# Kernel tuning notes

Measured on AMD Instinct MI355X. Metric: run time of the kernel, lower is better.

The kernel has to match this reference:

```python
import jax, jax.numpy as jnp
import numpy as np

INPUT_DIM = 512
PROJ_DIM = 128
HIDDEN = INPUT_DIM // 2  # 256


def setup_inputs() -> dict:
    key = jax.random.key(0)
    ks = jax.random.split(key, 6)
    B = 8192
    s1 = 1.0 / np.sqrt(INPUT_DIM)
    s2 = 1.0 / np.sqrt(HIDDEN)
    return {
        "fused_text": jax.random.normal(ks[0], (B, INPUT_DIM), dtype=jnp.float32),
        "x": jax.random.normal(ks[1], (B, INPUT_DIM), dtype=jnp.float32),
        # generator layer 1: Linear(input_dim, input_dim//2), torch layout [out, in]
        "W1": jax.random.uniform(ks[2], (HIDDEN, INPUT_DIM), jnp.float32, -s1, s1),
        "b1": jax.random.uniform(ks[3], (HIDDEN,), jnp.float32, -s1, s1),
        # generator layer 2: Linear(input_dim//2, proj_dim * input_dim)
        "W2": jax.random.uniform(ks[4], (PROJ_DIM * INPUT_DIM, HIDDEN), jnp.float32, -s2, s2),
        "b2": jax.random.uniform(ks[5], (PROJ_DIM * INPUT_DIM,), jnp.float32, -s2, s2),
    }


def reference(fused_text, x, W1, b1, W2, b2):
    B = fused_text.shape[0]
    # hypernetwork generator MLP
    h = jax.nn.relu(fused_text @ W1.T + b1)          # [B, hidden]
    w_flat = h @ W2.T + b2                           # [B, proj_dim * input_dim]
    W = w_flat.reshape(B, PROJ_DIM, INPUT_DIM)       # per-sample weights
    # per-sample projection: bmm(W, x[..., None]).squeeze(-1)
    out = jnp.einsum("bpi,bi->bp", W, x)             # [B, proj_dim]
    return out
```

## Files before the change

### kernel.cpp

```cpp
#include <hip/hip_runtime.h>
#include <stdint.h>

#define B_SZ   8192
#define IN_DIM 512
#define HID    256
#define PROJ   128

typedef __attribute__((ext_vector_type(8))) short bf16x8;
typedef __attribute__((ext_vector_type(4))) float f32x4;

#define GLDS16(gp, lp) __builtin_amdgcn_global_load_lds( \
    (const __attribute__((address_space(1))) void*)(gp), \
    (__attribute__((address_space(3))) void*)(lp), 16, 0, 0)

__device__ __forceinline__ unsigned short f2bf(float f) {
    union { float f; uint32_t u; } c; c.f = f;
    uint32_t u = c.u;
    uint32_t r = (u + 0x7fffu + ((u >> 16) & 1u)) >> 16;
    return (unsigned short)r;
}
__device__ __forceinline__ float bfhi(uint32_t v) {
    union { uint32_t u; float f; } c; c.u = v & 0xffff0000u; return c.f;
}
__device__ __forceinline__ float bflo(uint32_t v) {
    union { uint32_t u; float f; } c; c.u = v << 16; return c.f;
}

__global__ __launch_bounds__(256) void k0_prep(
        const float4* __restrict__ W2, ushort4* __restrict__ W2b,
        const float* __restrict__ x, unsigned short* __restrict__ xTb) {
    __shared__ float tile[64][65];
    const int bid = blockIdx.x;
    if (bid < 2048) {
        const int nW2 = (PROJ * IN_DIM * HID) / 4;
        const int stride = 2048 * 256;
        for (int i = bid * 256 + threadIdx.x; i < nW2; i += stride) {
            float4 v = W2[i];
            ushort4 o;
            o.x = f2bf(v.x); o.y = f2bf(v.y); o.z = f2bf(v.z); o.w = f2bf(v.w);
            W2b[i] = o;
        }
    } else {
        const int tb = bid - 2048;
        const int bi = tb & 7, bb = tb >> 3;
        const int i0 = bi * 64, b0 = bb * 64;
        const int t = threadIdx.x;
        const int c = t & 63, r4 = t >> 6;
        #pragma unroll
        for (int rr = 0; rr < 64; rr += 4)
            tile[rr + r4][c] = x[(size_t)(b0 + rr + r4) * IN_DIM + i0 + c];
        __syncthreads();
        #pragma unroll
        for (int rr = 0; rr < 64; rr += 4)
            xTb[(size_t)(i0 + rr + r4) * B_SZ + b0 + c] = f2bf(tile[c][rr + r4]);
    }
}

__device__ __forceinline__ bf16x8 ld_cvt8(const float* __restrict__ s) {
    float4 a = *(const float4*)s;
    float4 b = *(const float4*)(s + 4);
    bf16x8 r;
    r[0] = (short)f2bf(a.x); r[1] = (short)f2bf(a.y);
    r[2] = (short)f2bf(a.z); r[3] = (short)f2bf(a.w);
    r[4] = (short)f2bf(b.x); r[5] = (short)f2bf(b.y);
    r[6] = (short)f2bf(b.z); r[7] = (short)f2bf(b.w);
    return r;
}

__global__ __launch_bounds__(256) void k1_hidden(
        const float* __restrict__ ft,
        const float* __restrict__ W1,
        const float* __restrict__ b1,
        unsigned short* __restrict__ hb) {
    const int lane = threadIdx.x & 63;
    const int wv   = threadIdx.x >> 6;
    const int l15  = lane & 15, q = lane >> 4;
    const int b0 = blockIdx.x * 64;
    const int n0 = wv * 64;

    f32x4 acc[4][4];
    const f32x4 z4 = {0.f, 0.f, 0.f, 0.f};
    #pragma unroll
    for (int mt = 0; mt < 4; ++mt)
        #pragma unroll
        for (int nt = 0; nt < 4; ++nt) acc[mt][nt] = z4;

    for (int kq = 0; kq < 16; ++kq) {
        const int koff = kq * 32 + q * 8;
        bf16x8 a[4], bb[4];
        #pragma unroll
        for (int mt = 0; mt < 4; ++mt)
            a[mt] = ld_cvt8(ft + (size_t)(b0 + mt*16 + l15) * IN_DIM + koff);
        #pragma unroll
        for (int nt = 0; nt < 4; ++nt)
            bb[nt] = ld_cvt8(W1 + (size_t)(n0 + nt*16 + l15) * IN_DIM + koff);
        #pragma unroll
        for (int mt = 0; mt < 4; ++mt)
            #pragma unroll
            for (int nt = 0; nt < 4; ++nt)
                acc[mt][nt] = __builtin_amdgcn_mfma_f32_16x16x32_bf16(
                    a[mt], bb[nt], acc[mt][nt], 0, 0, 0);
    }
    #pragma unroll
    for (int nt = 0; nt < 4; ++nt) {
        float bias = b1[n0 + nt*16 + l15];
        #pragma unroll
        for (int mt = 0; mt < 4; ++mt)
            #pragma unroll
            for (int r = 0; r < 4; ++r) {
                float v = acc[mt][nt][r] + bias;
                v = fmaxf(v, 0.f);
                hb[(size_t)(b0 + mt*16 + q*4 + r) * HID + n0 + nt*16 + l15] = f2bf(v);
            }
    }
}

__global__ __launch_bounds__(256, 4) void k3_main(
        const unsigned short* __restrict__ W2b,
        const unsigned short* __restrict__ hb,
        const unsigned short* __restrict__ xTb,
        const float* __restrict__ b2,
        float* __restrict__ out) {
    __shared__ unsigned short lbs[2][64 * 128];
    const int tid  = threadIdx.x;
    const int lane = tid & 63;
    const int wv   = tid >> 6;
    const int l15  = lane & 15, q = lane >> 4;
    const int pgrp = blockIdx.x & 63;
    const int bsup = blockIdx.x >> 6;
    const int p0   = pgrp * 2;
    const int b0w  = bsup * 128 + wv * 32;
    const f32x4 z4 = {0.f, 0.f, 0.f, 0.f};

    const int grow_sub = lane >> 4;
    const int cbase    = (lane & 15) ^ grow_sub;

    const int qx   = q ^ (l15 & 3);
    const int kbit = (l15 >> 2) & 1;

    float oacc[2][2][4];
    #pragma unroll
    for (int pp = 0; pp < 2; ++pp)
        #pragma unroll
        for (int mt = 0; mt < 2; ++mt)
            #pragma unroll
            for (int r = 0; r < 4; ++r) oacc[pp][mt][r] = 0.f;

    bf16x8 afr[2][4];

    {
        #pragma unroll
        for (int jj = 0; jj < 4; ++jj) {
            const int j   = wv * 4 + jj;
            const int row = j * 4 + grow_sub;
            const int p   = row >> 5, ir = row & 31;
            const int c   = cbase ^ (4 * (jj & 1));
            const unsigned short* g = W2b
                + ((size_t)(p0 + p) * IN_DIM + ir) * HID + c * 8;
            GLDS16(g, &lbs[0][j * 512]);
        }
    }

    #pragma unroll 1
    for (int t = 0; t < 32; ++t) {
        __syncthreads();

        if (t < 31) {
            const int tn = t + 1;
            const int kh = tn >> 4, i0 = (tn & 15) * 32;
            unsigned short* Ld = lbs[tn & 1];
            #pragma unroll
            for (int jj = 0; jj < 4; ++jj) {
                const int j   = wv * 4 + jj;
                const int row = j * 4 + grow_sub;
                const int p   = row >> 5, ir = row & 31;
                const int c   = cbase ^ (4 * (jj & 1));
                const unsigned short* g = W2b
                    + ((size_t)(p0 + p) * IN_DIM + i0 + ir) * HID + kh * 128 + c * 8;
                GLDS16(g, &Ld[j * 512]);
            }
        }

        const int kh = t >> 4;
        if ((t & 15) == 0) {
            #pragma unroll
            for (int mt = 0; mt < 2; ++mt) {
                const unsigned short* hrow =
                    hb + (size_t)(b0w + mt*16 + l15) * HID + kh * 128 + q * 8;
                #pragma unroll
                for (int kq = 0; kq < 4; ++kq)
                    afr[mt][kq] = *(const bf16x8*)(hrow + kq * 32);
            }
        }

        const unsigned short* Lb = lbs[t & 1];
        const int i0 = (t & 15) * 32;

        #pragma unroll
        for (int sub = 0; sub < 2; ++sub) {
            const int irow = i0 + sub * 16 + l15;
            uint2 xv[2];
            const unsigned short* xp = xTb + (size_t)irow * B_SZ + b0w + q * 4;
            #pragma unroll
            for (int mt = 0; mt < 2; ++mt)
                xv[mt] = *(const uint2*)(xp + mt * 16);

            const float b2v = (kh == 0) ? b2[p0 * 512 + irow] : 0.f;
            const float b2w = (kh == 0) ? b2[(p0 + 1) * 512 + irow] : 0.f;

            #pragma unroll
            for (int pp = 0; pp < 2; ++pp) {
                const unsigned short* Bp = Lb + (pp*32 + sub*16 + l15) * 128;
                bf16x8 bfr[4];
                #pragma unroll
                for (int kq = 0; kq < 4; ++kq) {
                    const int cpos = qx + 4 * (kq ^ kbit);
                    bfr[kq] = *(const bf16x8*)(Bp + cpos * 8);
                }

                f32x4 D[2];
                #pragma unroll
                for (int mt = 0; mt < 2; ++mt)
                    D[mt] = __builtin_amdgcn_mfma_f32_16x16x32_bf16(afr[mt][0], bfr[0], z4, 0, 0, 0);
                #pragma unroll
                for (int kq = 1; kq < 4; ++kq)
                    #pragma unroll
                    for (int mt = 0; mt < 2; ++mt)
                        D[mt] = __builtin_amdgcn_mfma_f32_16x16x32_bf16(afr[mt][kq], bfr[kq], D[mt], 0, 0, 0);

                const float bb = pp ? b2w : b2v;
                #pragma unroll
                for (int mt = 0; mt < 2; ++mt) {
                    oacc[pp][mt][0] = fmaf(D[mt][0] + bb, bflo(xv[mt].x), oacc[pp][mt][0]);
                    oacc[pp][mt][1] = fmaf(D[mt][1] + bb, bfhi(xv[mt].x), oacc[pp][mt][1]);
                    oacc[pp][mt][2] = fmaf(D[mt][2] + bb, bflo(xv[mt].y), oacc[pp][mt][2]);
                    oacc[pp][mt][3] = fmaf(D[mt][3] + bb, bfhi(xv[mt].y), oacc[pp][mt][3]);
                }
            }
        }
    }

    #pragma unroll
    for (int pp = 0; pp < 2; ++pp)
        #pragma unroll
        for (int mt = 0; mt < 2; ++mt)
            #pragma unroll
            for (int r = 0; r < 4; ++r) {
                float v = oacc[pp][mt][r];
                v += __shfl_xor(v, 1, 16);
                v += __shfl_xor(v, 2, 16);
                v += __shfl_xor(v, 4, 16);
                v += __shfl_xor(v, 8, 16);
                if (l15 == 0)
                    out[(size_t)(b0w + mt*16 + q*4 + r) * PROJ + p0 + pp] = v;
            }
}

extern "C" void kernel_launch(void* const* d_in, const int* in_sizes, int n_in,
                              void* d_out, int out_size, void* d_ws, size_t ws_size,
                              hipStream_t stream) {
    const float* ft = (const float*)d_in[0];
    const float* x  = (const float*)d_in[1];
    const float* W1 = (const float*)d_in[2];
    const float* b1 = (const float*)d_in[3];
    const float* W2 = (const float*)d_in[4];
    const float* b2 = (const float*)d_in[5];
    float* out = (float*)d_out;

    char* ws = (char*)d_ws;
    unsigned short* W2b = (unsigned short*)(ws);
    unsigned short* hb  = (unsigned short*)(ws + 33554432);
    unsigned short* xTb = (unsigned short*)(ws + 37748736);

    hipLaunchKernelGGL(k0_prep, dim3(3072), dim3(256), 0, stream,
        (const float4*)W2, (ushort4*)W2b, x, xTb);
    hipLaunchKernelGGL(k1_hidden, dim3(128), dim3(256), 0, stream, ft, W1, b1, hb);
    hipLaunchKernelGGL(k3_main, dim3(4096), dim3(256), 0, stream, W2b, hb, xTb, b2, out);
}
```

Baseline: 489.3 us.

## Hoist b2 bias term into separate x·B2 GEMM and enlarge main kernel batch tile

The b2 bias contribution is factored out algebraically as x @ reshape(b2, PROJ, IN_DIM)^T and computed by a new small MFMA kernel that writes the output first. The main kernel then accumulates into out with +=, dropping the per-row bias loads and adds. The main kernel's per-wave batch tile is doubled from 32 to 64 rows, with occupancy hint lowered from 4 to 3 and half the blocks, to reuse each LDS-staged W2 tile across more samples. k1 is also retiled to 32 rows per block with twice the grid. The trade is more registers per thread and an extra launch, plus a read-modify-write of out.

```diff
diff --git a/kernel.cpp b/kernel.cpp
--- a/kernel.cpp
+++ b/kernel.cpp
@@ -75,27 +75,27 @@
     const int lane = threadIdx.x & 63;
     const int wv   = threadIdx.x >> 6;
     const int l15  = lane & 15, q = lane >> 4;
-    const int b0 = blockIdx.x * 64;
+    const int b0 = blockIdx.x * 32;
     const int n0 = wv * 64;
 
-    f32x4 acc[4][4];
+    f32x4 acc[2][4];
     const f32x4 z4 = {0.f, 0.f, 0.f, 0.f};
     #pragma unroll
-    for (int mt = 0; mt < 4; ++mt)
+    for (int mt = 0; mt < 2; ++mt)
         #pragma unroll
         for (int nt = 0; nt < 4; ++nt) acc[mt][nt] = z4;
 
     for (int kq = 0; kq < 16; ++kq) {
         const int koff = kq * 32 + q * 8;
-        bf16x8 a[4], bb[4];
-        #pragma unroll
-        for (int mt = 0; mt < 4; ++mt)
+        bf16x8 a[2], bb[4];
+        #pragma unroll
+        for (int mt = 0; mt < 2; ++mt)
             a[mt] = ld_cvt8(ft + (size_t)(b0 + mt*16 + l15) * IN_DIM + koff);
         #pragma unroll
         for (int nt = 0; nt < 4; ++nt)
             bb[nt] = ld_cvt8(W1 + (size_t)(n0 + nt*16 + l15) * IN_DIM + koff);
         #pragma unroll
-        for (int mt = 0; mt < 4; ++mt)
+        for (int mt = 0; mt < 2; ++mt)
             #pragma unroll
             for (int nt = 0; nt < 4; ++nt)
                 acc[mt][nt] = __builtin_amdgcn_mfma_f32_16x16x32_bf16(
@@ -105,7 +105,7 @@
     for (int nt = 0; nt < 4; ++nt) {
         float bias = b1[n0 + nt*16 + l15];
         #pragma unroll
-        for (int mt = 0; mt < 4; ++mt)
+        for (int mt = 0; mt < 2; ++mt)
             #pragma unroll
             for (int r = 0; r < 4; ++r) {
                 float v = acc[mt][nt][r] + bias;
@@ -115,11 +115,53 @@
     }
 }
 
-__global__ __launch_bounds__(256, 4) void k3_main(
+__global__ __launch_bounds__(256) void k2_bias(
+        const float* __restrict__ x,
+        const float* __restrict__ b2,
+        float* __restrict__ out) {
+    const int lane = threadIdx.x & 63;
+    const int wv   = threadIdx.x >> 6;
+    const int l15  = lane & 15, q = lane >> 4;
+    const int b0 = blockIdx.x * 32;
+    const int n0 = wv * 32;
+
+    f32x4 acc[2][2];
+    const f32x4 z4 = {0.f, 0.f, 0.f, 0.f};
+    #pragma unroll
+    for (int mt = 0; mt < 2; ++mt)
+        #pragma unroll
+        for (int nt = 0; nt < 2; ++nt) acc[mt][nt] = z4;
+
+    for (int kq = 0; kq < 16; ++kq) {
+        const int koff = kq * 32 + q * 8;
+        bf16x8 a[2], bb[2];
+        #pragma unroll
+        for (int mt = 0; mt < 2; ++mt)
+            a[mt] = ld_cvt8(x + (size_t)(b0 + mt*16 + l15) * IN_DIM + koff);
+        #pragma unroll
+        for (int nt = 0; nt < 2; ++nt)
+            bb[nt] = ld_cvt8(b2 + (size_t)(n0 + nt*16 + l15) * IN_DIM + koff);
+        #pragma unroll
+        for (int mt = 0; mt < 2; ++mt)
+            #pragma unroll
+            for (int nt = 0; nt < 2; ++nt)
+                acc[mt][nt] = __builtin_amdgcn_mfma_f32_16x16x32_bf16(
+                    a[mt], bb[nt], acc[mt][nt], 0, 0, 0);
+    }
+    #pragma unroll
+    for (int mt = 0; mt < 2; ++mt)
+        #pragma unroll
+        for (int nt = 0; nt < 2; ++nt)
+            #pragma unroll
+            for (int r = 0; r < 4; ++r)
+                out[(size_t)(b0 + mt*16 + q*4 + r) * PROJ + n0 + nt*16 + l15]
+                    = acc[mt][nt][r];
+}
+
+__global__ __launch_bounds__(256, 3) void k3_main(
         const unsigned short* __restrict__ W2b,
         const unsigned short* __restrict__ hb,
         const unsigned short* __restrict__ xTb,
-        const float* __restrict__ b2,
         float* __restrict__ out) {
     __shared__ unsigned short lbs[2][64 * 128];
     const int tid  = threadIdx.x;
@@ -129,7 +171,7 @@
     const int pgrp = blockIdx.x & 63;
     const int bsup = blockIdx.x >> 6;
     const int p0   = pgrp * 2;
-    const int b0w  = bsup * 128 + wv * 32;
+    const int b0w  = bsup * 256 + wv * 64;
     const f32x4 z4 = {0.f, 0.f, 0.f, 0.f};
 
     const int grow_sub = lane >> 4;
@@ -138,15 +180,15 @@
     const int qx   = q ^ (l15 & 3);
     const int kbit = (l15 >> 2) & 1;
 
-    float oacc[2][2][4];
+    float oacc[2][4][4];
     #pragma unroll
     for (int pp = 0; pp < 2; ++pp)
         #pragma unroll
-        for (int mt = 0; mt < 2; ++mt)
+        for (int mt = 0; mt < 4; ++mt)
             #pragma unroll
             for (int r = 0; r < 4; ++r) oacc[pp][mt][r] = 0.f;
 
-    bf16x8 afr[2][4];
+    bf16x8 afr[4][4];
 
     {
         #pragma unroll
@@ -184,7 +226,7 @@
         const int kh = t >> 4;
         if ((t & 15) == 0) {
             #pragma unroll
-            for (int mt = 0; mt < 2; ++mt) {
+            for (int mt = 0; mt < 4; ++mt) {
                 const unsigned short* hrow =
                     hb + (size_t)(b0w + mt*16 + l15) * HID + kh * 128 + q * 8;
                 #pragma unroll
@@ -199,14 +241,11 @@
         #pragma unroll
         for (int sub = 0; sub < 2; ++sub) {
             const int irow = i0 + sub * 16 + l15;
-            uint2 xv[2];
+            uint2 xv[4];
             const unsigned short* xp = xTb + (size_t)irow * B_SZ + b0w + q * 4;
             #pragma unroll
-            for (int mt = 0; mt < 2; ++mt)
+            for (int mt = 0; mt < 4; ++mt)
                 xv[mt] = *(const uint2*)(xp + mt * 16);
-
-            const float b2v = (kh == 0) ? b2[p0 * 512 + irow] : 0.f;
-            const float b2w = (kh == 0) ? b2[(p0 + 1) * 512 + irow] : 0.f;
 
             #pragma unroll
             for (int pp = 0; pp < 2; ++pp) {
@@ -218,23 +257,22 @@
                     bfr[kq] = *(const bf16x8*)(Bp + cpos * 8);
                 }
 
-                f32x4 D[2];
-                #pragma unroll
-                for (int mt = 0; mt < 2; ++mt)
+                f32x4 D[4];
+                #pragma unroll
+                for (int mt = 0; mt < 4; ++mt)
                     D[mt] = __builtin_amdgcn_mfma_f32_16x16x32_bf16(afr[mt][0], bfr[0], z4, 0, 0, 0);
                 #pragma unroll
                 for (int kq = 1; kq < 4; ++kq)
                     #pragma unroll
-                    for (int mt = 0; mt < 2; ++mt)
+                    for (int mt = 0; mt < 4; ++mt)
                         D[mt] = __builtin_amdgcn_mfma_f32_16x16x32_bf16(afr[mt][kq], bfr[kq], D[mt], 0, 0, 0);
 
-                const float bb = pp ? b2w : b2v;
-                #pragma unroll
-                for (int mt = 0; mt < 2; ++mt) {
-                    oacc[pp][mt][0] = fmaf(D[mt][0] + bb, bflo(xv[mt].x), oacc[pp][mt][0]);
-                    oacc[pp][mt][1] = fmaf(D[mt][1] + bb, bfhi(xv[mt].x), oacc[pp][mt][1]);
-                    oacc[pp][mt][2] = fmaf(D[mt][2] + bb, bflo(xv[mt].y), oacc[pp][mt][2]);
-                    oacc[pp][mt][3] = fmaf(D[mt][3] + bb, bfhi(xv[mt].y), oacc[pp][mt][3]);
+                #pragma unroll
+                for (int mt = 0; mt < 4; ++mt) {
+                    oacc[pp][mt][0] = fmaf(D[mt][0], bflo(xv[mt].x), oacc[pp][mt][0]);
+                    oacc[pp][mt][1] = fmaf(D[mt][1], bfhi(xv[mt].x), oacc[pp][mt][1]);
+                    oacc[pp][mt][2] = fmaf(D[mt][2], bflo(xv[mt].y), oacc[pp][mt][2]);
+                    oacc[pp][mt][3] = fmaf(D[mt][3], bfhi(xv[mt].y), oacc[pp][mt][3]);
                 }
             }
         }
@@ -243,7 +281,7 @@
     #pragma unroll
     for (int pp = 0; pp < 2; ++pp)
         #pragma unroll
-        for (int mt = 0; mt < 2; ++mt)
+        for (int mt = 0; mt < 4; ++mt)
             #pragma unroll
             for (int r = 0; r < 4; ++r) {
                 float v = oacc[pp][mt][r];
@@ -251,8 +289,11 @@
                 v += __shfl_xor(v, 2, 16);
                 v += __shfl_xor(v, 4, 16);
                 v += __shfl_xor(v, 8, 16);
-                if (l15 == 0)
-                    out[(size_t)(b0w + mt*16 + q*4 + r) * PROJ + p0 + pp] = v;
+                if (l15 == 0) {
+                    const size_t idx =
+                        (size_t)(b0w + mt*16 + q*4 + r) * PROJ + p0 + pp;
+                    out[idx] += v;
+                }
             }
 }
 
@@ -274,6 +315,7 @@
 
     hipLaunchKernelGGL(k0_prep, dim3(3072), dim3(256), 0, stream,
         (const float4*)W2, (ushort4*)W2b, x, xTb);
-    hipLaunchKernelGGL(k1_hidden, dim3(128), dim3(256), 0, stream, ft, W1, b1, hb);
-    hipLaunchKernelGGL(k3_main, dim3(4096), dim3(256), 0, stream, W2b, hb, xTb, b2, out);
-}
+    hipLaunchKernelGGL(k1_hidden, dim3(256), dim3(256), 0, stream, ft, W1, b1, hb);
+    hipLaunchKernelGGL(k2_bias, dim3(256), dim3(256), 0, stream, x, b2, out);
+    hipLaunchKernelGGL(k3_main, dim3(2048), dim3(256), 0, stream, W2b, hb, xTb, out);
+}
```

Result: slower. 654.8 us (+33.8%).

## Factor b2 term into separate GEMM, retile main kernel, drop x transpose

Applied to the files above, without the earlier changes.

Splits the bias contribution b2·x out of the main loop into a small MFMA GEMM (k2_bias) that writes a transposed output buffer. The main kernel then accumulates into that buffer, and a final kernel transposes it to [B, PROJ]. The main kernel now covers 128 batch rows per wave with a 64-wide k chunk, and reads fp32 x directly instead of a pre-transposed bf16 copy, so the x transpose in prep goes away. This adds two kernel launches and a read-modify-write of outT. Occupancy drops to 3 blocks per SM, and the afr/xq register arrays are larger.

```diff
diff --git a/kernel.cpp b/kernel.cpp
--- a/kernel.cpp
+++ b/kernel.cpp
@@ -19,40 +19,16 @@
     uint32_t r = (u + 0x7fffu + ((u >> 16) & 1u)) >> 16;
     return (unsigned short)r;
 }
-__device__ __forceinline__ float bfhi(uint32_t v) {
-    union { uint32_t u; float f; } c; c.u = v & 0xffff0000u; return c.f;
-}
-__device__ __forceinline__ float bflo(uint32_t v) {
-    union { uint32_t u; float f; } c; c.u = v << 16; return c.f;
-}
 
 __global__ __launch_bounds__(256) void k0_prep(
-        const float4* __restrict__ W2, ushort4* __restrict__ W2b,
-        const float* __restrict__ x, unsigned short* __restrict__ xTb) {
-    __shared__ float tile[64][65];
-    const int bid = blockIdx.x;
-    if (bid < 2048) {
-        const int nW2 = (PROJ * IN_DIM * HID) / 4;
-        const int stride = 2048 * 256;
-        for (int i = bid * 256 + threadIdx.x; i < nW2; i += stride) {
-            float4 v = W2[i];
-            ushort4 o;
-            o.x = f2bf(v.x); o.y = f2bf(v.y); o.z = f2bf(v.z); o.w = f2bf(v.w);
-            W2b[i] = o;
-        }
-    } else {
-        const int tb = bid - 2048;
-        const int bi = tb & 7, bb = tb >> 3;
-        const int i0 = bi * 64, b0 = bb * 64;
-        const int t = threadIdx.x;
-        const int c = t & 63, r4 = t >> 6;
-        #pragma unroll
-        for (int rr = 0; rr < 64; rr += 4)
-            tile[rr + r4][c] = x[(size_t)(b0 + rr + r4) * IN_DIM + i0 + c];
-        __syncthreads();
-        #pragma unroll
-        for (int rr = 0; rr < 64; rr += 4)
-            xTb[(size_t)(i0 + rr + r4) * B_SZ + b0 + c] = f2bf(tile[c][rr + r4]);
+        const float4* __restrict__ W2, ushort4* __restrict__ W2b) {
+    const int nW2 = (PROJ * IN_DIM * HID) / 4;
+    const int stride = 2048 * 256;
+    for (int i = blockIdx.x * 256 + threadIdx.x; i < nW2; i += stride) {
+        float4 v = W2[i];
+        ushort4 o;
+        o.x = f2bf(v.x); o.y = f2bf(v.y); o.z = f2bf(v.z); o.w = f2bf(v.w);
+        W2b[i] = o;
     }
 }
 
@@ -75,27 +51,27 @@
     const int lane = threadIdx.x & 63;
     const int wv   = threadIdx.x >> 6;
     const int l15  = lane & 15, q = lane >> 4;
-    const int b0 = blockIdx.x * 64;
+    const int b0 = blockIdx.x * 32;
     const int n0 = wv * 64;
 
-    f32x4 acc[4][4];
+    f32x4 acc[2][4];
     const f32x4 z4 = {0.f, 0.f, 0.f, 0.f};
     #pragma unroll
-    for (int mt = 0; mt < 4; ++mt)
+    for (int mt = 0; mt < 2; ++mt)
         #pragma unroll
         for (int nt = 0; nt < 4; ++nt) acc[mt][nt] = z4;
 
     for (int kq = 0; kq < 16; ++kq) {
         const int koff = kq * 32 + q * 8;
-        bf16x8 a[4], bb[4];
-        #pragma unroll
-        for (int mt = 0; mt < 4; ++mt)
+        bf16x8 a[2], bb[4];
+        #pragma unroll
+        for (int mt = 0; mt < 2; ++mt)
             a[mt] = ld_cvt8(ft + (size_t)(b0 + mt*16 + l15) * IN_DIM + koff);
         #pragma unroll
         for (int nt = 0; nt < 4; ++nt)
             bb[nt] = ld_cvt8(W1 + (size_t)(n0 + nt*16 + l15) * IN_DIM + koff);
         #pragma unroll
-        for (int mt = 0; mt < 4; ++mt)
+        for (int mt = 0; mt < 2; ++mt)
             #pragma unroll
             for (int nt = 0; nt < 4; ++nt)
                 acc[mt][nt] = __builtin_amdgcn_mfma_f32_16x16x32_bf16(
@@ -105,7 +81,7 @@
     for (int nt = 0; nt < 4; ++nt) {
         float bias = b1[n0 + nt*16 + l15];
         #pragma unroll
-        for (int mt = 0; mt < 4; ++mt)
+        for (int mt = 0; mt < 2; ++mt)
             #pragma unroll
             for (int r = 0; r < 4; ++r) {
                 float v = acc[mt][nt][r] + bias;
@@ -115,13 +91,55 @@
     }
 }
 
-__global__ __launch_bounds__(256, 4) void k3_main(
+__global__ __launch_bounds__(256) void k2_bias(
+        const float* __restrict__ x,
+        const float* __restrict__ b2,
+        float* __restrict__ outT) {
+    const int lane = threadIdx.x & 63;
+    const int wv   = threadIdx.x >> 6;
+    const int l15  = lane & 15, q = lane >> 4;
+    const int b0 = blockIdx.x * 64;
+    const int pw = wv * 32;
+
+    f32x4 acc[2][4];
+    const f32x4 z4 = {0.f, 0.f, 0.f, 0.f};
+    #pragma unroll
+    for (int pt = 0; pt < 2; ++pt)
+        #pragma unroll
+        for (int bb = 0; bb < 4; ++bb) acc[pt][bb] = z4;
+
+    for (int kq = 0; kq < 16; ++kq) {
+        const int koff = kq * 32 + q * 8;
+        bf16x8 a[2], bx[4];
+        #pragma unroll
+        for (int pt = 0; pt < 2; ++pt)
+            a[pt] = ld_cvt8(b2 + (size_t)(pw + pt*16 + l15) * IN_DIM + koff);
+        #pragma unroll
+        for (int bb = 0; bb < 4; ++bb)
+            bx[bb] = ld_cvt8(x + (size_t)(b0 + bb*16 + l15) * IN_DIM + koff);
+        #pragma unroll
+        for (int pt = 0; pt < 2; ++pt)
+            #pragma unroll
+            for (int bb = 0; bb < 4; ++bb)
+                acc[pt][bb] = __builtin_amdgcn_mfma_f32_16x16x32_bf16(
+                    a[pt], bx[bb], acc[pt][bb], 0, 0, 0);
+    }
+    #pragma unroll
+    for (int pt = 0; pt < 2; ++pt)
+        #pragma unroll
+        for (int bb = 0; bb < 4; ++bb)
+            #pragma unroll
+            for (int r = 0; r < 4; ++r)
+                outT[(size_t)(pw + pt*16 + q*4 + r) * B_SZ + b0 + bb*16 + l15]
+                    = acc[pt][bb][r];
+}
+
+__global__ __launch_bounds__(256, 3) void k3_main(
         const unsigned short* __restrict__ W2b,
         const unsigned short* __restrict__ hb,
-        const unsigned short* __restrict__ xTb,
-        const float* __restrict__ b2,
-        float* __restrict__ out) {
-    __shared__ unsigned short lbs[2][64 * 128];
+        const float* __restrict__ x,
+        float* __restrict__ outT) {
+    __shared__ unsigned short lbs[2][64 * 64];
     const int tid  = threadIdx.x;
     const int lane = tid & 63;
     const int wv   = tid >> 6;
@@ -129,112 +147,87 @@
     const int pgrp = blockIdx.x & 63;
     const int bsup = blockIdx.x >> 6;
     const int p0   = pgrp * 2;
-    const int b0w  = bsup * 128 + wv * 32;
+    const int b0w  = bsup * 512 + wv * 128;
     const f32x4 z4 = {0.f, 0.f, 0.f, 0.f};
 
-    const int grow_sub = lane >> 4;
-    const int cbase    = (lane & 15) ^ grow_sub;
-
-    const int qx   = q ^ (l15 & 3);
-    const int kbit = (l15 >> 2) & 1;
-
-    float oacc[2][2][4];
+    const int grow = lane >> 3;
+    const int gchk = lane & 7;
+
+    const unsigned short* gsrc[2];
+    #pragma unroll
+    for (int jj = 0; jj < 2; ++jj) {
+        const int r = wv*16 + jj*8 + grow;
+        const int c = gchk ^ (r & 7);
+        gsrc[jj] = W2b + ((size_t)(p0 + (r >> 5)) * IN_DIM + (r & 31)) * HID + c * 8;
+    }
+
+    float oacc[2][8];
     #pragma unroll
     for (int pp = 0; pp < 2; ++pp)
         #pragma unroll
-        for (int mt = 0; mt < 2; ++mt)
-            #pragma unroll
-            for (int r = 0; r < 4; ++r) oacc[pp][mt][r] = 0.f;
-
-    bf16x8 afr[2][4];
-
-    {
-        #pragma unroll
-        for (int jj = 0; jj < 4; ++jj) {
-            const int j   = wv * 4 + jj;
-            const int row = j * 4 + grow_sub;
-            const int p   = row >> 5, ir = row & 31;
-            const int c   = cbase ^ (4 * (jj & 1));
-            const unsigned short* g = W2b
-                + ((size_t)(p0 + p) * IN_DIM + ir) * HID + c * 8;
-            GLDS16(g, &lbs[0][j * 512]);
-        }
-    }
+        for (int bt = 0; bt < 8; ++bt) oacc[pp][bt] = 0.f;
+
+    bf16x8 afr[8][2];
+
+    const unsigned short* hbase = hb + (size_t)(b0w + l15) * HID + q * 8;
+    const float* xbase = x + (size_t)(b0w + l15) * IN_DIM + q * 4;
+
+    #pragma unroll
+    for (int jj = 0; jj < 2; ++jj)
+        GLDS16(gsrc[jj], &lbs[0][(wv*16 + jj*8) * 64]);
 
     #pragma unroll 1
-    for (int t = 0; t < 32; ++t) {
+    for (int t = 0; t < 64; ++t) {
         __syncthreads();
 
-        if (t < 31) {
+        if (t < 63) {
             const int tn = t + 1;
-            const int kh = tn >> 4, i0 = (tn & 15) * 32;
+            const int khn = tn >> 4, icn = tn & 15;
             unsigned short* Ld = lbs[tn & 1];
             #pragma unroll
-            for (int jj = 0; jj < 4; ++jj) {
-                const int j   = wv * 4 + jj;
-                const int row = j * 4 + grow_sub;
-                const int p   = row >> 5, ir = row & 31;
-                const int c   = cbase ^ (4 * (jj & 1));
-                const unsigned short* g = W2b
-                    + ((size_t)(p0 + p) * IN_DIM + i0 + ir) * HID + kh * 128 + c * 8;
-                GLDS16(g, &Ld[j * 512]);
+            for (int jj = 0; jj < 2; ++jj)
+                GLDS16(gsrc[jj] + (size_t)icn * 32 * HID + khn * 64,
+                       &Ld[(wv*16 + jj*8) * 64]);
+        }
+
+        const int kh = t >> 4;
+        const int ic = t & 15;
+        if ((t & 15) == 0) {
+            #pragma unroll
+            for (int bt = 0; bt < 8; ++bt) {
+                const unsigned short* hrow = hbase + bt * 16 * HID + kh * 64;
+                afr[bt][0] = *(const bf16x8*)(hrow);
+                afr[bt][1] = *(const bf16x8*)(hrow + 32);
             }
         }
 
-        const int kh = t >> 4;
-        if ((t & 15) == 0) {
-            #pragma unroll
-            for (int mt = 0; mt < 2; ++mt) {
-                const unsigned short* hrow =
-                    hb + (size_t)(b0w + mt*16 + l15) * HID + kh * 128 + q * 8;
+        const unsigned short* Lb = lbs[t & 1];
+
+        #pragma unroll
+        for (int sub = 0; sub < 2; ++sub) {
+            float4 xq[8];
+            #pragma unroll
+            for (int bt = 0; bt < 8; ++bt)
+                xq[bt] = *(const float4*)(xbase + (size_t)bt * 16 * IN_DIM
+                                          + ic * 32 + sub * 16);
+            #pragma unroll
+            for (int pp = 0; pp < 2; ++pp) {
+                const int trow = pp*32 + sub*16 + l15;
+                const int sw = trow & 7;
+                bf16x8 wf0 = *(const bf16x8*)(&Lb[trow*64 + ((q)     ^ sw) * 8]);
+                bf16x8 wf1 = *(const bf16x8*)(&Lb[trow*64 + ((4 + q) ^ sw) * 8]);
                 #pragma unroll
-                for (int kq = 0; kq < 4; ++kq)
-                    afr[mt][kq] = *(const bf16x8*)(hrow + kq * 32);
-            }
-        }
-
-        const unsigned short* Lb = lbs[t & 1];
-        const int i0 = (t & 15) * 32;
-
-        #pragma unroll
-        for (int sub = 0; sub < 2; ++sub) {
-            const int irow = i0 + sub * 16 + l15;
-            uint2 xv[2];
-            const unsigned short* xp = xTb + (size_t)irow * B_SZ + b0w + q * 4;
-            #pragma unroll
-            for (int mt = 0; mt < 2; ++mt)
-                xv[mt] = *(const uint2*)(xp + mt * 16);
-
-            const float b2v = (kh == 0) ? b2[p0 * 512 + irow] : 0.f;
-            const float b2w = (kh == 0) ? b2[(p0 + 1) * 512 + irow] : 0.f;
-
-            #pragma unroll
-            for (int pp = 0; pp < 2; ++pp) {
-                const unsigned short* Bp = Lb + (pp*32 + sub*16 + l15) * 128;
-                bf16x8 bfr[4];
-                #pragma unroll
-                for (int kq = 0; kq < 4; ++kq) {
-                    const int cpos = qx + 4 * (kq ^ kbit);
-                    bfr[kq] = *(const bf16x8*)(Bp + cpos * 8);
-                }
-
-                f32x4 D[2];
-                #pragma unroll
-                for (int mt = 0; mt < 2; ++mt)
-                    D[mt] = __builtin_amdgcn_mfma_f32_16x16x32_bf16(afr[mt][0], bfr[0], z4, 0, 0, 0);
-                #pragma unroll
-                for (int kq = 1; kq < 4; ++kq)
-                    #pragma unroll
-                    for (int mt = 0; mt < 2; ++mt)
-                        D[mt] = __builtin_amdgcn_mfma_f32_16x16x32_bf16(afr[mt][kq], bfr[kq], D[mt], 0, 0, 0);
-
-                const float bb = pp ? b2w : b2v;
-                #pragma unroll
-                for (int mt = 0; mt < 2; ++mt) {
-                    oacc[pp][mt][0] = fmaf(D[mt][0] + bb, bflo(xv[mt].x), oacc[pp][mt][0]);
-                    oacc[pp][mt][1] = fmaf(D[mt][1] + bb, bfhi(xv[mt].x), oacc[pp][mt][1]);
-                    oacc[pp][mt][2] = fmaf(D[mt][2] + bb, bflo(xv[mt].y), oacc[pp][mt][2]);
-                    oacc[pp][mt][3] = fmaf(D[mt][3] + bb, bfhi(xv[mt].y), oacc[pp][mt][3]);
+                for (int bt = 0; bt < 8; ++bt) {
+                    f32x4 D = __builtin_amdgcn_mfma_f32_16x16x32_bf16(
+                        wf0, afr[bt][0], z4, 0, 0, 0);
+                    D = __builtin_amdgcn_mfma_f32_16x16x32_bf16(
+                        wf1, afr[bt][1], D, 0, 0, 0);
+                    float v = oacc[pp][bt];
+                    v = fmaf(D[0], xq[bt].x, v);
+                    v = fmaf(D[1], xq[bt].y, v);
+                    v = fmaf(D[2], xq[bt].z, v);
+                    v = fmaf(D[3], xq[bt].w, v);
+                    oacc[pp][bt] = v;
                 }
             }
         }
@@ -243,17 +236,30 @@
     #pragma unroll
     for (int pp = 0; pp < 2; ++pp)
         #pragma unroll
-        for (int mt = 0; mt < 2; ++mt)
-            #pragma unroll
-            for (int r = 0; r < 4; ++r) {
-                float v = oacc[pp][mt][r];
-                v += __shfl_xor(v, 1, 16);
-                v += __shfl_xor(v, 2, 16);
-                v += __shfl_xor(v, 4, 16);
-                v += __shfl_xor(v, 8, 16);
-                if (l15 == 0)
-                    out[(size_t)(b0w + mt*16 + q*4 + r) * PROJ + p0 + pp] = v;
-            }
+        for (int bt = 0; bt < 8; ++bt) {
+            float v = oacc[pp][bt];
+            v += __shfl_xor(v, 16, 64);
+            v += __shfl_xor(v, 32, 64);
+            if (lane < 16)
+                outT[(size_t)(p0 + pp) * B_SZ + b0w + bt*16 + lane] += v;
+        }
+}
+
+__global__ __launch_bounds__(256) void k4_tr(
+        const float* __restrict__ outT, float* __restrict__ out) {
+    __shared__ float tile[64][65];
+    const int pb = blockIdx.x & 1;
+    const int bb = blockIdx.x >> 1;
+    const int p0 = pb * 64, b0 = bb * 64;
+    const int t = threadIdx.x;
+    const int c = t & 63, r4 = t >> 6;
+    #pragma unroll
+    for (int rr = 0; rr < 64; rr += 4)
+        tile[rr + r4][c] = outT[(size_t)(p0 + rr + r4) * B_SZ + b0 + c];
+    __syncthreads();
+    #pragma unroll
+    for (int rr = 0; rr < 64; rr += 4)
+        out[(size_t)(b0 + rr + r4) * PROJ + p0 + c] = tile[c][rr + r4];
 }
 
 extern "C" void kernel_launch(void* const* d_in, const int* in_sizes, int n_in,
@@ -270,10 +276,12 @@
     char* ws = (char*)d_ws;
     unsigned short* W2b = (unsigned short*)(ws);
     unsigned short* hb  = (unsigned short*)(ws + 33554432);
-    unsigned short* xTb = (unsigned short*)(ws + 37748736);
-
-    hipLaunchKernelGGL(k0_prep, dim3(3072), dim3(256), 0, stream,
-        (const float4*)W2, (ushort4*)W2b, x, xTb);
-    hipLaunchKernelGGL(k1_hidden, dim3(128), dim3(256), 0, stream, ft, W1, b1, hb);
-    hipLaunchKernelGGL(k3_main, dim3(4096), dim3(256), 0, stream, W2b, hb, xTb, b2, out);
-}
+    float*          oT  = (float*)(ws + 37748736);
+
+    hipLaunchKernelGGL(k0_prep, dim3(2048), dim3(256), 0, stream,
+        (const float4*)W2, (ushort4*)W2b);
+    hipLaunchKernelGGL(k1_hidden, dim3(256), dim3(256), 0, stream, ft, W1, b1, hb);
+    hipLaunchKernelGGL(k2_bias, dim3(128), dim3(256), 0, stream, x, b2, oT);
+    hipLaunchKernelGGL(k3_main, dim3(1024), dim3(256), 0, stream, W2b, hb, x, oT);
+    hipLaunchKernelGGL(k4_tr, dim3(256), dim3(256), 0, stream, oT, out);
+}
```

Measured after the change: 761.9 us. 1.56x slower.
